# Kernel tuning notes

Measured on AMD Instinct MI355X. Metric: run time of the kernel, lower is better.

## Reference

```python
import jax, jax.numpy as jnp
import numpy as np

B, S, H, I = 4, 2048, 2048, 8192
LN_EPS = 1e-6  # DeepSpeed inference layer-norm epsilon


def setup_inputs() -> dict:
    key = jax.random.key(0)
    ks = jax.random.split(key, 10)
    return {
        "input": jax.random.normal(ks[0], (B, S, H), dtype=jnp.float32),
        "residual": jax.random.normal(ks[1], (B, S, H), dtype=jnp.float32),
        "residual_norm": jax.random.normal(ks[2], (B, S, H), dtype=jnp.float32),
        "bias": jax.random.normal(ks[3], (H,), dtype=jnp.float32) * 0.02,
        "gamma": jnp.ones((H,), dtype=jnp.float32) + jax.random.normal(ks[4], (H,), dtype=jnp.float32) * 0.02,
        "beta": jax.random.normal(ks[5], (H,), dtype=jnp.float32) * 0.02,
        "inter_w": jax.random.normal(ks[6], (H, I), dtype=jnp.float32) * 0.02,
        "inter_b": jax.random.normal(ks[7], (I,), dtype=jnp.float32) * 0.02,
        "output_w": jax.random.normal(ks[8], (I, H), dtype=jnp.float32) * 0.02,
        "output_b": jax.random.normal(ks[9], (H,), dtype=jnp.float32) * 0.02,
    }


def reference(input, residual, residual_norm, bias, gamma, beta,
              inter_w, inter_b, output_w, output_b):
    # --- mlp_gemm_func (pre-LN path, attn_nw is not None) ---
    # Fused: residual_add = attention_output + attention_bias + residual
    residual_add = input + residual + bias                    # [B,S,H]
    # LayerNorm over hidden dim
    mu = jnp.mean(residual_add, axis=-1, keepdims=True)
    var = jnp.mean(jnp.square(residual_add - mu), axis=-1, keepdims=True)
    ln = (residual_add - mu) * jax.lax.rsqrt(var + LN_EPS) * gamma + beta
    # GEMM + bias + GeLU, then second GEMM
    h = jax.nn.gelu(jnp.einsum("bsh,hi->bsi", ln, inter_w) + inter_b,
                    approximate=False)                        # [B,S,I]
    out = jnp.einsum("bsi,ih->bsh", h, output_w)              # [B,S,H]
    # --- residual_add_func (pre-LN, mlp_after_attn): mlp_out + residual_add + final_bias ---
    return out + residual_add + output_b
```

## Files before the change

kernel.cpp:

```cpp
#include <hip/hip_runtime.h>

typedef __attribute__((ext_vector_type(8))) __bf16 bf16x8;
typedef __attribute__((ext_vector_type(4))) float f32x4;

#define AS1(p) ((const __attribute__((address_space(1))) void*)(uintptr_t)(p))
#define AS3(p) ((__attribute__((address_space(3))) void*)(uint32_t)(uintptr_t)(p))
#define GLD16(gp, lp) __builtin_amdgcn_global_load_lds(AS1(gp), AS3(lp), 16, 0, 0)

static constexpr int Bb = 4, Ss = 2048, Hh = 2048, Ih = 8192;
static constexpr int Mm = Bb * Ss;

__device__ __forceinline__ float gelu_exact(float x) {
    return 0.5f * x * (1.0f + erff(x * 0.70710678118654752440f));
}

__global__ __launch_bounds__(256) void transpose_cvt(const float* __restrict__ src,
                                                     __bf16* __restrict__ dst,
                                                     int R, int C) {
    __shared__ float tile[32][33];
    const int tx = threadIdx.x, ty = threadIdx.y;
    const int cB = blockIdx.x * 32, rB = blockIdx.y * 32;
#pragma unroll
    for (int i = 0; i < 4; ++i)
        tile[ty + i * 8][tx] = src[(size_t)(rB + ty + i * 8) * C + cB + tx];
    __syncthreads();
#pragma unroll
    for (int i = 0; i < 4; ++i)
        dst[(size_t)(cB + ty + i * 8) * R + rB + tx] = (__bf16)tile[tx][ty + i * 8];
}

__global__ __launch_bounds__(256) void fused_ln(const float* __restrict__ input,
                                                const float* __restrict__ residual,
                                                const float* __restrict__ bias,
                                                const float* __restrict__ gamma,
                                                const float* __restrict__ beta,
                                                __bf16* __restrict__ lnb,
                                                __bf16* __restrict__ rab) {
    const int row = blockIdx.x;
    const int tid = threadIdx.x;
    const size_t base = (size_t)row * Hh;
    const int e = tid * 8;

    float4 x0 = *(const float4*)(input + base + e);
    float4 x1 = *(const float4*)(input + base + e + 4);
    float4 r0 = *(const float4*)(residual + base + e);
    float4 r1 = *(const float4*)(residual + base + e + 4);
    float4 b0 = *(const float4*)(bias + e);
    float4 b1 = *(const float4*)(bias + e + 4);

    float s[8];
    s[0] = x0.x + r0.x + b0.x; s[1] = x0.y + r0.y + b0.y;
    s[2] = x0.z + r0.z + b0.z; s[3] = x0.w + r0.w + b0.w;
    s[4] = x1.x + r1.x + b1.x; s[5] = x1.y + r1.y + b1.y;
    s[6] = x1.z + r1.z + b1.z; s[7] = x1.w + r1.w + b1.w;

    float sum = 0.f, sq = 0.f;
#pragma unroll
    for (int j = 0; j < 8; ++j) { sum += s[j]; sq += s[j] * s[j]; }
#pragma unroll
    for (int o = 32; o > 0; o >>= 1) {
        sum += __shfl_xor(sum, o);
        sq  += __shfl_xor(sq, o);
    }
    __shared__ float red[8];
    const int wv = tid >> 6, ln_ = tid & 63;
    if (ln_ == 0) { red[wv] = sum; red[4 + wv] = sq; }
    __syncthreads();
    sum = red[0] + red[1] + red[2] + red[3];
    sq  = red[4] + red[5] + red[6] + red[7];

    const float mu   = sum * (1.0f / Hh);
    const float var  = sq * (1.0f / Hh) - mu * mu;
    const float rstd = rsqrtf(var + 1e-6f);

    float4 g0 = *(const float4*)(gamma + e);
    float4 g1 = *(const float4*)(gamma + e + 4);
    float4 t0 = *(const float4*)(beta + e);
    float4 t1 = *(const float4*)(beta + e + 4);
    float g[8] = {g0.x, g0.y, g0.z, g0.w, g1.x, g1.y, g1.z, g1.w};
    float t[8] = {t0.x, t0.y, t0.z, t0.w, t1.x, t1.y, t1.z, t1.w};

    bf16x8 lv, rv;
#pragma unroll
    for (int j = 0; j < 8; ++j) {
        rv[j] = (__bf16)s[j];
        lv[j] = (__bf16)((s[j] - mu) * rstd * g[j] + t[j]);
    }
    *(bf16x8*)(lnb + base + e) = lv;
    *(bf16x8*)(rab + base + e) = rv;
}


#define CFENCE asm volatile("" ::: "memory")
#define BAR()  do { CFENCE; __builtin_amdgcn_s_barrier(); CFENCE; } while (0)
#define SP1 __builtin_amdgcn_s_setprio(1)
#define SP0 __builtin_amdgcn_s_setprio(0)
#define VM8 asm volatile("s_waitcnt vmcnt(8)" ::: "memory")
#define VM4 asm volatile("s_waitcnt vmcnt(4)" ::: "memory")
#define VM0 asm volatile("s_waitcnt vmcnt(0)" ::: "memory")
#define NOPS ((void)0)

__device__ __forceinline__ void ldA4(const char* p0, const char* p1, const int mhOff,
                                     bf16x8 (&af)[4][2]) {
#pragma unroll
    for (int m = 0; m < 4; ++m) {
        af[m][0] = *(const bf16x8*)(p0 + mhOff + m * 2048);
        af[m][1] = *(const bf16x8*)(p1 + mhOff + m * 2048);
    }
}
__device__ __forceinline__ void ldB2(const char* p0, const char* p1, const int nhOff,
                                     bf16x8 (&bf)[2][2]) {
#pragma unroll
    for (int n = 0; n < 2; ++n) {
        bf[n][0] = *(const bf16x8*)(p0 + nhOff + n * 2048);
        bf[n][1] = *(const bf16x8*)(p1 + nhOff + n * 2048);
    }
}
template <int MH, int NH>
__device__ __forceinline__ void mfmaQ(const bf16x8 (&a)[4][2], const bf16x8 (&b)[2][2],
                                      f32x4 (&acc)[8][4]) {
#pragma unroll
    for (int m = 0; m < 4; ++m)
#pragma unroll
        for (int n = 0; n < 2; ++n)
#pragma unroll
            for (int ks = 0; ks < 2; ++ks)
                acc[MH * 4 + m][NH * 2 + n] = __builtin_amdgcn_mfma_f32_16x16x32_bf16(
                    a[m][ks], b[n][ks], acc[MH * 4 + m][NH * 2 + n], 0, 0, 0);
}
__device__ __forceinline__ void stage2(const __bf16* src, __bf16* dst, const size_t row64) {
    GLD16(src, dst);
    GLD16(src + row64, dst + 4096);
}

template <int MODE>
__global__ __launch_bounds__(512, 2) void gemm256(const __bf16* __restrict__ A,
                                                  const __bf16* __restrict__ Bt,
                                                  const float* __restrict__ bias,
                                                  const __bf16* __restrict__ rab,
                                                  __bf16* __restrict__ outH,
                                                  float* __restrict__ outF,
                                                  int M, int N, int K) {
    __shared__ __align__(128) __bf16 lds[2 * 4 * 128 * 64];

    const int tid = threadIdx.x;
    const int nbx = N >> 8;
    const int nwg = gridDim.x;
    const int cpx = nwg >> 3;
    const int bid = blockIdx.x;
    const int swz = (bid & 7) * cpx + (bid >> 3);
    const int by = swz / nbx, bx = swz - by * nbx;
    const int mBase = by << 8, nBase = bx << 8;

    const int wave = tid >> 6, lane = tid & 63;
    const int wr = wave >> 2, wc = wave & 3;

    const int NT = K >> 6;
    const int NI = NT >> 1;

    char* ldsc = (char*)lds;
    const int laneCol0 = (((lane >> 4) << 4)) ^ ((lane & 7) << 4);
    const int laneCol1 = laneCol0 ^ 64;
    const int aLaneR = (lane & 15) << 7;
    const int bLaneR = (((wc & 1) << 6) + (lane & 15)) << 7;
    const char* pA[2][2] = {
        {ldsc + (0 * 4 + wr) * 16384 + aLaneR + laneCol0,
         ldsc + (0 * 4 + wr) * 16384 + aLaneR + laneCol1},
        {ldsc + (1 * 4 + wr) * 16384 + aLaneR + laneCol0,
         ldsc + (1 * 4 + wr) * 16384 + aLaneR + laneCol1}};
    const char* pB[2][2] = {
        {ldsc + (0 * 4 + 2 + (wc >> 1)) * 16384 + bLaneR + laneCol0,
         ldsc + (0 * 4 + 2 + (wc >> 1)) * 16384 + bLaneR + laneCol1},
        {ldsc + (1 * 4 + 2 + (wc >> 1)) * 16384 + bLaneR + laneCol0,
         ldsc + (1 * 4 + 2 + (wc >> 1)) * 16384 + bLaneR + laneCol1}};

    const int srow = tid >> 3;
    const int scol = ((tid & 7) ^ (srow & 7)) << 3;
    const __bf16* aSt = A + (size_t)(mBase + srow) * K + scol;
    const __bf16* bSt = Bt + (size_t)(nBase + srow) * K + scol;
    __bf16* lw = lds + tid * 8;
    const size_t row64 = (size_t)64 * K;
    const size_t row128 = (size_t)128 * K;

#define STA(buf, h, t) stage2(aSt + (h) * row128 + (size_t)(t) * 64, lw + ((buf) * 4 + (h)) * 8192, row64)
#define STB(buf, h, t) stage2(bSt + (h) * row128 + (size_t)(t) * 64, lw + ((buf) * 4 + 2 + (h)) * 8192, row64)
#define STGB(P, T) do { STB(P, 0, T); STB(P, 1, T); } while (0)
#define STGA(P, T) do { STA(P, 0, T); STA(P, 1, T); } while (0)
#define RDN(NP) do { ldB2(pB[NP][0], pB[NP][1], 0, b0v); \
                     ldA4(pA[NP][0], pA[NP][1], 0, a0v); } while (0)

    f32x4 acc[8][4] = {};
    bf16x8 a0v[4][2], a1v[4][2], b0v[2][2], b1v[2][2];

    STGB(0, 0); STGA(0, 0);
    STGB(1, 1); STGA(1, 1);
    VM8;
    BAR();
    RDN(0);

#define TILE(P, NP, STAGEB, GATE, STAGEA, NEXTRD)          \
    SP1; mfmaQ<0, 0>(a0v, b0v, acc); SP0;                  \
    ldB2(pB[P][0], pB[P][1], 4096, b1v);                   \
    SP1; mfmaQ<0, 1>(a0v, b1v, acc); SP0;                  \
    ldA4(pA[P][0], pA[P][1], 8192, a1v);                   \
    BAR();                                                 \
    SP1; mfmaQ<1, 1>(a1v, b1v, acc); SP0;                  \
    STAGEB;                                                \
    GATE;                                                  \
    BAR();                                                 \
    SP1; mfmaQ<1, 0>(a1v, b0v, acc); SP0;                  \
    NEXTRD;                                                \
    STAGEA;

    for (int i = 0; i < NI - 1; ++i) {
        const int t2a = 2 * i + 2, t2b = 2 * i + 3;
        TILE(0, 1, STGB(0, t2a), VM4, STGA(0, t2a), RDN(1))
        TILE(1, 0, STGB(1, t2b), VM4, STGA(1, t2b), RDN(0))
    }
    TILE(0, 1, NOPS, VM0, NOPS, RDN(1))
    TILE(1, 0, NOPS, NOPS, NOPS, NOPS)
#undef TILE

    const int r0 = mBase + wr * 128 + ((lane >> 4) << 2);
    const int c0 = nBase + wc * 64 + (lane & 15);
    float bb[4];
#pragma unroll
    for (int nf = 0; nf < 4; ++nf) bb[nf] = bias[c0 + nf * 16];
#pragma unroll
    for (int mf = 0; mf < 8; ++mf) {
        const int row = r0 + mf * 16;
#pragma unroll
        for (int nf = 0; nf < 4; ++nf) {
            const int col = c0 + nf * 16;
#pragma unroll
            for (int j = 0; j < 4; ++j) {
                const size_t idx = (size_t)(row + j) * N + col;
                const float v = acc[mf][nf][j] + bb[nf];
                if (MODE == 0) {
                    outH[idx] = (__bf16)gelu_exact(v);
                } else {
                    outF[idx] = v + (float)rab[idx];
                }
            }
        }
    }
#undef STA
#undef STB
#undef STGB
#undef STGA
#undef RDN
}

extern "C" void kernel_launch(void* const* d_in, const int* in_sizes, int n_in,
                              void* d_out, int out_size, void* d_ws, size_t ws_size,
                              hipStream_t stream) {
    const float* input    = (const float*)d_in[0];
    const float* residual = (const float*)d_in[1];
    const float* bias     = (const float*)d_in[3];
    const float* gamma    = (const float*)d_in[4];
    const float* beta     = (const float*)d_in[5];
    const float* inter_w  = (const float*)d_in[6];
    const float* inter_b  = (const float*)d_in[7];
    const float* output_w = (const float*)d_in[8];
    const float* output_b = (const float*)d_in[9];
    float* out = (float*)d_out;

    __bf16* w1t  = (__bf16*)d_ws;
    __bf16* w2t  = w1t + (size_t)Ih * Hh;
    __bf16* lnb  = w2t + (size_t)Hh * Ih;
    __bf16* rab  = lnb + (size_t)Mm * Hh;
    __bf16* hbuf = rab + (size_t)Mm * Hh;

    transpose_cvt<<<dim3(Ih / 32, Hh / 32), dim3(32, 8), 0, stream>>>(inter_w, w1t, Hh, Ih);
    transpose_cvt<<<dim3(Hh / 32, Ih / 32), dim3(32, 8), 0, stream>>>(output_w, w2t, Ih, Hh);

    fused_ln<<<Mm, 256, 0, stream>>>(input, residual, bias, gamma, beta, lnb, rab);

    gemm256<0><<<dim3((Mm / 256) * (Ih / 256)), 512, 0, stream>>>(
        lnb, w1t, inter_b, nullptr, hbuf, nullptr, Mm, Ih, Hh);

    gemm256<1><<<dim3((Mm / 256) * (Hh / 256)), 512, 0, stream>>>(
        hbuf, w2t, output_b, rab, nullptr, out, Mm, Hh, Ih);
}
```

Baseline: 731.8 us.

## Reschedule GEMM main loop with explicit lgkmcnt waits and rotating B fragments

Rewrites the double-buffered bf16 MFMA main loop so LDS fragment reads for the next quarter are issued before the current MFMA block, gated by explicit s_waitcnt lgkmcnt counts instead of implicit compiler waits. The LDS layout is regrouped so all A buffers are contiguous and all B buffers follow them, and B fragments rotate between two register sets across tiles. The intent is to overlap LDS reads with MFMA work more tightly. In exchange it drains vmcnt to zero before a barrier every tile, which may expose global-load latency that the old partial vmcnt wait hid.

```diff
diff --git a/kernel.cpp b/kernel.cpp
--- a/kernel.cpp
+++ b/kernel.cpp
@@ -92,28 +92,27 @@
 
 
 #define CFENCE asm volatile("" ::: "memory")
-#define BAR()  do { CFENCE; __builtin_amdgcn_s_barrier(); CFENCE; } while (0)
+#define BAR_   do { CFENCE; __builtin_amdgcn_s_barrier(); CFENCE; } while (0)
 #define SP1 __builtin_amdgcn_s_setprio(1)
 #define SP0 __builtin_amdgcn_s_setprio(0)
+#define LGK(n) asm volatile("s_waitcnt lgkmcnt(" #n ")" ::: "memory")
+#define VM0 asm volatile("s_waitcnt vmcnt(0)" ::: "memory")
 #define VM8 asm volatile("s_waitcnt vmcnt(8)" ::: "memory")
-#define VM4 asm volatile("s_waitcnt vmcnt(4)" ::: "memory")
-#define VM0 asm volatile("s_waitcnt vmcnt(0)" ::: "memory")
-#define NOPS ((void)0)
-
-__device__ __forceinline__ void ldA4(const char* p0, const char* p1, const int mhOff,
-                                     bf16x8 (&af)[4][2]) {
+
+__device__ __forceinline__ void rdA(bf16x8 (&d)[4][2], const char* a0, const char* a1,
+                                    const int off) {
 #pragma unroll
     for (int m = 0; m < 4; ++m) {
-        af[m][0] = *(const bf16x8*)(p0 + mhOff + m * 2048);
-        af[m][1] = *(const bf16x8*)(p1 + mhOff + m * 2048);
-    }
-}
-__device__ __forceinline__ void ldB2(const char* p0, const char* p1, const int nhOff,
-                                     bf16x8 (&bf)[2][2]) {
+        d[m][0] = *(const bf16x8*)(a0 + off + m * 2048);
+        d[m][1] = *(const bf16x8*)(a1 + off + m * 2048);
+    }
+}
+__device__ __forceinline__ void rdB(bf16x8 (&d)[2][2], const char* b0, const char* b1,
+                                    const int off) {
 #pragma unroll
     for (int n = 0; n < 2; ++n) {
-        bf[n][0] = *(const bf16x8*)(p0 + nhOff + n * 2048);
-        bf[n][1] = *(const bf16x8*)(p1 + nhOff + n * 2048);
+        d[n][0] = *(const bf16x8*)(b0 + off + n * 2048);
+        d[n][1] = *(const bf16x8*)(b1 + off + n * 2048);
     }
 }
 template <int MH, int NH>
@@ -161,18 +160,12 @@
     char* ldsc = (char*)lds;
     const int laneCol0 = (((lane >> 4) << 4)) ^ ((lane & 7) << 4);
     const int laneCol1 = laneCol0 ^ 64;
-    const int aLaneR = (lane & 15) << 7;
-    const int bLaneR = (((wc & 1) << 6) + (lane & 15)) << 7;
-    const char* pA[2][2] = {
-        {ldsc + (0 * 4 + wr) * 16384 + aLaneR + laneCol0,
-         ldsc + (0 * 4 + wr) * 16384 + aLaneR + laneCol1},
-        {ldsc + (1 * 4 + wr) * 16384 + aLaneR + laneCol0,
-         ldsc + (1 * 4 + wr) * 16384 + aLaneR + laneCol1}};
-    const char* pB[2][2] = {
-        {ldsc + (0 * 4 + 2 + (wc >> 1)) * 16384 + bLaneR + laneCol0,
-         ldsc + (0 * 4 + 2 + (wc >> 1)) * 16384 + bLaneR + laneCol1},
-        {ldsc + (1 * 4 + 2 + (wc >> 1)) * 16384 + bLaneR + laneCol0,
-         ldsc + (1 * 4 + 2 + (wc >> 1)) * 16384 + bLaneR + laneCol1}};
+    const int aOff = wr * 16384 + ((lane & 15) << 7);
+    const int bOff = 65536 + (wc >> 1) * 16384 + ((((wc & 1) << 6) + (lane & 15)) << 7);
+    const char* aRd0 = ldsc + aOff + laneCol0;
+    const char* aRd1 = ldsc + aOff + laneCol1;
+    const char* bRd0 = ldsc + bOff + laneCol0;
+    const char* bRd1 = ldsc + bOff + laneCol1;
 
     const int srow = tid >> 3;
     const int scol = ((tid & 7) ^ (srow & 7)) << 3;
@@ -182,43 +175,45 @@
     const size_t row64 = (size_t)64 * K;
     const size_t row128 = (size_t)128 * K;
 
-#define STA(buf, h, t) stage2(aSt + (h) * row128 + (size_t)(t) * 64, lw + ((buf) * 4 + (h)) * 8192, row64)
-#define STB(buf, h, t) stage2(bSt + (h) * row128 + (size_t)(t) * 64, lw + ((buf) * 4 + 2 + (h)) * 8192, row64)
-#define STGB(P, T) do { STB(P, 0, T); STB(P, 1, T); } while (0)
-#define STGA(P, T) do { STA(P, 0, T); STA(P, 1, T); } while (0)
-#define RDN(NP) do { ldB2(pB[NP][0], pB[NP][1], 0, b0v); \
-                     ldA4(pA[NP][0], pA[NP][1], 0, a0v); } while (0)
+#define STA(buf, h, t) stage2(aSt + (h) * row128 + (size_t)(t) * 64, lw + ((buf) * 2 + (h)) * 8192, row64)
+#define STB(buf, h, t) stage2(bSt + (h) * row128 + (size_t)(t) * 64, lw + 32768 + ((buf) * 2 + (h)) * 8192, row64)
 
     f32x4 acc[8][4] = {};
-    bf16x8 a0v[4][2], a1v[4][2], b0v[2][2], b1v[2][2];
-
-    STGB(0, 0); STGA(0, 0);
-    STGB(1, 1); STGA(1, 1);
+    bf16x8 aLo[4][2], aHi[4][2], bE[2][2], bO[2][2];
+
+    STA(0, 0, 0); STA(0, 1, 0); STB(0, 0, 0); STB(0, 1, 0);
+    STA(1, 0, 1); STA(1, 1, 1); STB(1, 0, 1); STB(1, 1, 1);
     VM8;
-    BAR();
-    RDN(0);
-
-#define TILE(P, NP, STAGEB, GATE, STAGEA, NEXTRD)          \
-    SP1; mfmaQ<0, 0>(a0v, b0v, acc); SP0;                  \
-    ldB2(pB[P][0], pB[P][1], 4096, b1v);                   \
-    SP1; mfmaQ<0, 1>(a0v, b1v, acc); SP0;                  \
-    ldA4(pA[P][0], pA[P][1], 8192, a1v);                   \
-    BAR();                                                 \
-    SP1; mfmaQ<1, 1>(a1v, b1v, acc); SP0;                  \
-    STAGEB;                                                \
-    GATE;                                                  \
-    BAR();                                                 \
-    SP1; mfmaQ<1, 0>(a1v, b0v, acc); SP0;                  \
-    NEXTRD;                                                \
-    STAGEA;
+    BAR_;
+    rdA(aLo, aRd0, aRd1, 0);
+    rdB(bE, bRd0, bRd1, 0);
+
+#define TILE(P, NP, BLO, BHI, HS, HN, T2)                                      \
+                                                \
+    rdB(BHI, bRd0, bRd1, (P) * 32768 + 4096);                                  \
+    LGK(4); SP1; mfmaQ<0, 0>(aLo, BLO, acc); SP0;                              \
+                                                \
+    rdA(aHi, aRd0, aRd1, (P) * 32768 + 8192);                                  \
+    LGK(8); SP1; mfmaQ<0, 1>(aLo, BHI, acc); SP0;                              \
+    VM0; BAR_;         \
+                             \
+    if (HS) { STB(P, 0, T2); STB(P, 1, T2); }                                  \
+    if (HN) rdA(aLo, aRd0, aRd1, (NP) * 32768);                                \
+    if (HN) { LGK(8); } else { LGK(0); }                                       \
+    SP1; mfmaQ<1, 1>(aHi, BHI, acc); SP0;                                      \
+    BAR_;                                  \
+               \
+    if (HS) { STA(P, 0, T2); STA(P, 1, T2); }                                  \
+    if (HN) rdB(BHI, bRd0, bRd1, (NP) * 32768);                                \
+    if (HN) { LGK(12); } else { LGK(0); }                                      \
+    SP1; mfmaQ<1, 0>(aHi, BLO, acc); SP0;
 
     for (int i = 0; i < NI - 1; ++i) {
-        const int t2a = 2 * i + 2, t2b = 2 * i + 3;
-        TILE(0, 1, STGB(0, t2a), VM4, STGA(0, t2a), RDN(1))
-        TILE(1, 0, STGB(1, t2b), VM4, STGA(1, t2b), RDN(0))
-    }
-    TILE(0, 1, NOPS, VM0, NOPS, RDN(1))
-    TILE(1, 0, NOPS, NOPS, NOPS, NOPS)
+        TILE(0, 1, bE, bO, true, true, 2 * i + 2)
+        TILE(1, 0, bO, bE, true, true, 2 * i + 3)
+    }
+    TILE(0, 1, bE, bO, false, true, 0)
+    TILE(1, 0, bO, bE, false, false, 0)
 #undef TILE
 
     const int r0 = mBase + wr * 128 + ((lane >> 4) << 2);
@@ -246,9 +241,6 @@
     }
 #undef STA
 #undef STB
-#undef STGB
-#undef STGA
-#undef RDN
 }
 
 extern "C" void kernel_launch(void* const* d_in, const int* in_sizes, int n_in,
```

New measurement: 1.899 ms. 160% more time.
